# Optimization experiments

Measured on AMD Instinct MI355X. Metric: run time of the kernel, lower is better.

The kernel has to match this reference:

```python
import jax, jax.numpy as jnp
import numpy as np

B, L, C, H, W = 2, 3, 64, 32, 32
DI, N, DT_RANK, K = 128, 16, 4, 4  # d_inner=2*C, d_state, dt_rank=ceil(C/16), 4 scan dirs


def setup_inputs() -> dict:
    key = jax.random.key(0)
    ks = iter(jax.random.split(key, 48))
    nrm = lambda shape, s=0.02: jax.random.normal(next(ks), shape, jnp.float32) * s
    return {
        "image_sequence": jax.random.normal(next(ks), (B, L, C, H, W), jnp.float32),
        "difficult_zone": jax.random.normal(next(ks), (B, C, H, W), jnp.float32),
        "sigma": jax.random.uniform(next(ks), (B, C, H, W), jnp.float32),
        # LayerNorm2d applied to each frame
        "norm_g": jnp.ones((C,)), "norm_b": jnp.zeros((C,)),
        # ConvolutionalResBlock (in=3C -> out=C), GroupNorm(num_groups=1)
        "gn1_g": jnp.ones((3 * C,)), "gn1_b": jnp.zeros((3 * C,)),
        "conv1_w": nrm((C, 3 * C, 3, 3)), "conv1_b": jnp.zeros((C,)),
        "gn2_g": jnp.ones((C,)), "gn2_b": jnp.zeros((C,)),
        "conv2_w": nrm((C, C, 3, 3)), "conv2_b": jnp.zeros((C,)),
        "skip_w": nrm((C, 3 * C, 1, 1)), "skip_b": jnp.zeros((C,)),
        # VSSBlock pre-norms
        "ln1_g": jnp.ones((C,)), "ln1_b": jnp.zeros((C,)),
        "ln2_g": jnp.ones((C,)), "ln2_b": jnp.zeros((C,)),
        # SS2D
        "in_proj_w": nrm((2 * DI, C)),
        "dwconv_w": nrm((DI, 1, 3, 3)), "dwconv_b": jnp.zeros((DI,)),
        "x_proj_w": nrm((K, DT_RANK + 2 * N, DI)),
        "dt_proj_w": nrm((K, DI, DT_RANK), 0.1),
        "dt_proj_b": jnp.log(jnp.expm1(jnp.full((K, DI), 0.01, jnp.float32))),
        "A_logs": jnp.log(jnp.tile(jnp.arange(1, N + 1, dtype=jnp.float32), (K * DI, 1))),
        "Ds": jnp.ones((K * DI,)),
        "out_norm_g": jnp.ones((DI,)), "out_norm_b": jnp.zeros((DI,)),
        "out_proj_w": nrm((C, DI)),
        # Mlp (hidden = C)
        "fc1_w": nrm((C, C)), "fc1_b": jnp.zeros((C,)),
        "fc2_w": nrm((C, C)), "fc2_b": jnp.zeros((C,)),
    }


def _ln(x, g, b, eps=1e-5):  # layernorm over last axis
    m = x.mean(-1, keepdims=True)
    v = x.var(-1, keepdims=True)
    return (x - m) * jax.lax.rsqrt(v + eps) * g + b


def _ln2d(x, g, b, eps=1e-6):  # per-pixel channel layernorm, NCHW
    m = x.mean(1, keepdims=True)
    v = x.var(1, keepdims=True)
    return (x - m) * jax.lax.rsqrt(v + eps) * g[None, :, None, None] + b[None, :, None, None]


def _gn1(x, g, b, eps=1e-5):  # GroupNorm(num_groups=1), NCHW
    m = x.mean((1, 2, 3), keepdims=True)
    v = x.var((1, 2, 3), keepdims=True)
    return (x - m) * jax.lax.rsqrt(v + eps) * g[None, :, None, None] + b[None, :, None, None]


def _conv(x, w, b, pad):
    y = jax.lax.conv_general_dilated(x, w, (1, 1), [(pad, pad), (pad, pad)],
                                     dimension_numbers=("NCHW", "OIHW", "NCHW"))
    return y + b[None, :, None, None]


def _forward(image_sequence, difficult_zone, sigma, norm_g, norm_b, gn1_g, gn1_b,
             conv1_w, conv1_b, gn2_g, gn2_b, conv2_w, conv2_b, skip_w, skip_b,
             ln1_g, ln1_b, ln2_g, ln2_b, in_proj_w, dwconv_w, dwconv_b, x_proj_w,
             dt_proj_w, dt_proj_b, A_logs, Ds, out_norm_g, out_norm_b, out_proj_w,
             fc1_w, fc1_b, fc2_w, fc2_b):
    b, l, c, h, w = image_sequence.shape
    bl, L2 = b * l, h * w
    # fold frame loop into batch (identical math per frame in the torch loop)
    frames = _ln2d(image_sequence.reshape(bl, c, h, w), norm_g, norm_b)
    dz = jnp.broadcast_to(difficult_zone[:, None], (b, l, c, h, w)).reshape(bl, c, h, w)
    sg = jnp.broadcast_to(sigma[:, None], (b, l, c, h, w)).reshape(bl, c, h, w)
    x = jnp.concatenate([dz, frames, sg], axis=1)  # [bl, 3c, h, w]
    # channel compressor: pre-act conv res block
    hdn = _conv(jax.nn.silu(_gn1(x, gn1_g, gn1_b)), conv1_w, conv1_b, 1)
    hdn = _conv(jax.nn.silu(_gn1(hdn, gn2_g, gn2_b)), conv2_w, conv2_b, 1)
    x = hdn + _conv(x, skip_w, skip_b, 0)          # [bl, c, h, w]
    x = x.transpose(0, 2, 3, 1)                    # [bl, h, w, c]
    # --- VSSBlock (pre-norm): x = x + SS2D(LN(x)) ---
    xn = _ln(x, ln1_g, ln1_b)
    xz = xn @ in_proj_w.T                          # [bl,h,w,2*DI]
    xc, z = jnp.split(xz, 2, axis=-1)
    xc = xc.transpose(0, 3, 1, 2)                  # [bl, DI, h, w]
    xc = jax.lax.conv_general_dilated(xc, dwconv_w, (1, 1), [(1, 1), (1, 1)],
                                      dimension_numbers=("NCHW", "OIHW", "NCHW"),
                                      feature_group_count=DI) + dwconv_b[None, :, None, None]
    xc = jax.nn.silu(xc)
    # 4-direction scan inputs (HW, WH, and their reverses)
    xf = xc.reshape(bl, DI, L2)
    xt = xc.transpose(0, 1, 3, 2).reshape(bl, DI, L2)
    xs = jnp.stack([xf, xt], axis=1)
    xs = jnp.concatenate([xs, jnp.flip(xs, axis=-1)], axis=1)  # [bl, 4, DI, L2]
    x_dbl = jnp.einsum("bkdl,kcd->bkcl", xs, x_proj_w)
    dts, Bs, Cs = jnp.split(x_dbl, [DT_RANK, DT_RANK + N], axis=2)
    dts = jnp.einsum("bkrl,kdr->bkdl", dts, dt_proj_w) + dt_proj_b[None, :, :, None]
    dts = jax.nn.softplus(dts)                     # [bl, 4, DI, L2]
    A = -jnp.exp(A_logs).reshape(K, DI, N)
    dA = jnp.exp(dts[..., None] * A[None, :, :, None, :])            # [bl,4,DI,L2,N]
    dBu = dts[..., None] * Bs.transpose(0, 1, 3, 2)[:, :, None] * xs[..., None]
    a_t = dA.transpose(3, 0, 1, 2, 4)              # [L2, bl, 4, DI, N]
    bu_t = dBu.transpose(3, 0, 1, 2, 4)
    c_t = Cs.transpose(3, 0, 1, 2)                 # [L2, bl, 4, N]

    def step(hid, inp):
        a_i, bu_i, c_i = inp
        hid = a_i * hid + bu_i
        return hid, jnp.einsum("bkdn,bkn->bkd", hid, c_i)

    h0 = jnp.zeros((bl, K, DI, N), xs.dtype)
    _, ys = jax.lax.scan(step, h0, (a_t, bu_t, c_t))                 # [L2, bl, 4, DI]
    ys = ys.transpose(1, 2, 3, 0) + xs * Ds.reshape(K, DI)[None, :, :, None]
    inv = jnp.flip(ys[:, 2:4], axis=-1)
    y = (ys[:, 0] + inv[:, 0]
         + ys[:, 1].reshape(bl, DI, w, h).transpose(0, 1, 3, 2).reshape(bl, DI, L2)
         + inv[:, 1].reshape(bl, DI, w, h).transpose(0, 1, 3, 2).reshape(bl, DI, L2))
    y = _ln(y.transpose(0, 2, 1), out_norm_g, out_norm_b).reshape(bl, h, w, DI)
    y = y * jax.nn.silu(z)
    x = x + y @ out_proj_w.T
    # --- x = x + Mlp(LN(x)) ---
    xn = _ln(x, ln2_g, ln2_b)
    x = x + (jax.nn.gelu(xn @ fc1_w.T + fc1_b, approximate=False) @ fc2_w.T + fc2_b)
    return x.transpose(0, 3, 1, 2).reshape(b, l, c, h, w)


def reference(image_sequence, difficult_zone, sigma, norm_g, norm_b, gn1_g, gn1_b,
              conv1_w, conv1_b, gn2_g, gn2_b, conv2_w, conv2_b, skip_w, skip_b,
              ln1_g, ln1_b, ln2_g, ln2_b, in_proj_w, dwconv_w, dwconv_b, x_proj_w,
              dt_proj_w, dt_proj_b, A_logs, Ds, out_norm_g, out_norm_b, out_proj_w,
              fc1_w, fc1_b, fc2_w, fc2_b):
    return _forward(image_sequence, difficult_zone, sigma, norm_g, norm_b, gn1_g, gn1_b,
                    conv1_w, conv1_b, gn2_g, gn2_b, conv2_w, conv2_b, skip_w, skip_b,
                    ln1_g, ln1_b, ln2_g, ln2_b, in_proj_w, dwconv_w, dwconv_b, x_proj_w,
                    dt_proj_w, dt_proj_b, A_logs, Ds, out_norm_g, out_norm_b, out_proj_w,
                    fc1_w, fc1_b, fc2_w, fc2_b)
```

## Files before the change

kernel.cpp:

```cpp
#include <hip/hip_runtime.h>
#include <math.h>

#define BL    6
#define CCH   64
#define C3    192
#define L2    1024
#define DIC   128
#define NST   16
#define K4    4
#define PSTR  1088
#define NCH   32

#define LOG2E 1.44269504088896340736f
#define LN2C  0.69314718055994530942f

__device__ __forceinline__ float fexp(float x){ return __builtin_amdgcn_exp2f(x*LOG2E); }
__device__ __forceinline__ float fsilu(float x){ return x * __builtin_amdgcn_rcpf(1.f + fexp(-x)); }
__device__ __forceinline__ float fsoftplus(float x){
  if (x > 20.f) return x;
  return __builtin_amdgcn_logf(1.f + fexp(x)) * LN2C;
}
__device__ __forceinline__ float fgelu(float x){
  return 0.5f*x*(1.f + erff(x*0.70710678118654752440f));
}

__global__ __launch_bounds__(256) void k_ln2d(const float* __restrict__ img,
    const float* __restrict__ dz, const float* __restrict__ sg,
    const float* __restrict__ g, const float* __restrict__ b, float* __restrict__ x3c,
    float* __restrict__ psum1, float* __restrict__ psq1){
  __shared__ float ps[4][16], pq[4][16], gs[4], gq[4];
  int s = blockIdx.x >> 6;
  int pg = blockIdx.x & 63;
  int tid = threadIdx.x;
  int px = tid & 15; int cg = tid >> 4;
  int wv = tid >> 6; int lane = tid & 63;
  int p = pg*16 + px;
  int bsmp = s/3;
  const float* fr = img + (size_t)s*CCH*L2;
  float vals[4]; float sm=0.f, sq=0.f;
  #pragma unroll
  for (int j=0;j<4;++j){
    int c = cg*4 + j;
    float v = fr[c*L2 + p];
    vals[j]=v; sm+=v; sq+=v*v;
  }
  sm += __shfl_xor(sm,16,64); sq += __shfl_xor(sq,16,64);
  sm += __shfl_xor(sm,32,64); sq += __shfl_xor(sq,32,64);
  if (lane < 16){ ps[wv][lane]=sm; pq[wv][lane]=sq; }
  __syncthreads();
  sm = ps[0][px]+ps[1][px]+ps[2][px]+ps[3][px];
  sq = pq[0][px]+pq[1][px]+pq[2][px]+pq[3][px];
  float mean = sm*(1.f/CCH); float var = sq*(1.f/CCH)-mean*mean;
  float rs = rsqrtf(var + 1e-6f);
  float* o = x3c + (size_t)s*C3*L2;
  const float* dzp = dz + (size_t)bsmp*CCH*L2;
  const float* sgp = sg + (size_t)bsmp*CCH*L2;
  float gsm=0.f, gsq=0.f;
  #pragma unroll
  for (int j=0;j<4;++j){
    int c = cg*4+j;
    float dzv = dzp[c*L2+p];
    float nv  = (vals[j]-mean)*rs*g[c] + b[c];
    float sgv = sgp[c*L2+p];
    o[c*L2+p] = dzv;
    o[(CCH+c)*L2+p] = nv;
    o[(2*CCH+c)*L2+p] = sgv;
    gsm += dzv+nv+sgv; gsq += dzv*dzv+nv*nv+sgv*sgv;
  }
  for (int m=1;m<64;m<<=1){ gsm+=__shfl_xor(gsm,m,64); gsq+=__shfl_xor(gsq,m,64); }
  if (lane==0){ gs[wv]=gsm; gq[wv]=gsq; }
  __syncthreads();
  if (tid==0){
    psum1[blockIdx.x] = gs[0]+gs[1]+gs[2]+gs[3];
    psq1 [blockIdx.x] = gq[0]+gq[1]+gq[2]+gq[3];
  }
}

__global__ __launch_bounds__(256) void k_gnact_pad(const float* __restrict__ x,
    const float* __restrict__ psum, const float* __restrict__ psq,
    const float* __restrict__ g, const float* __restrict__ b,
    int ch, int parts, float inv_n, float eps, float* __restrict__ out){
  int bx = blockIdx.x;
  int s = bx / ch; int c = bx % ch;
  int tid = threadIdx.x;
  float sm=0.f, sq=0.f;
  for (int i=0;i<parts;++i){ sm += psum[s*parts+i]; sq += psq[s*parts+i]; }
  float mean = sm*inv_n;
  float var = sq*inv_n - mean*mean;
  float rs = rsqrtf(var + eps);
  float gc = g[c]*rs; float bc = b[c] - mean*rs*g[c];
  float4 v = *(const float4*)(x + (size_t)bx*1024 + tid*4);
  float4 o; o.x = fsilu(v.x*gc+bc); o.y = fsilu(v.y*gc+bc);
  o.z = fsilu(v.z*gc+bc); o.w = fsilu(v.w*gc+bc);
  float* pl = out + (size_t)bx*PSTR;
  *(float4*)(pl + 32 + tid*4) = o;
  float4 z4 = make_float4(0.f,0.f,0.f,0.f);
  if (tid < 8)  *(float4*)(pl + tid*4) = z4;
  else if (tid < 16) *(float4*)(pl + 1056 + (tid-8)*4) = z4;
}

__device__ __forceinline__ void conv_row_acc(float4& a0, float4& a1, float4 mid, float lf, float rt,
    const float* wp0, const float* wp1){
  float w0=wp0[0], w1=wp0[1], w2=wp0[2];
  a0.x = fmaf(w0,lf,   fmaf(w1,mid.x, fmaf(w2,mid.y, a0.x)));
  a0.y = fmaf(w0,mid.x,fmaf(w1,mid.y, fmaf(w2,mid.z, a0.y)));
  a0.z = fmaf(w0,mid.y,fmaf(w1,mid.z, fmaf(w2,mid.w, a0.z)));
  a0.w = fmaf(w0,mid.z,fmaf(w1,mid.w, fmaf(w2,rt,    a0.w)));
  float v0=wp1[0], v1=wp1[1], v2=wp1[2];
  a1.x = fmaf(v0,lf,   fmaf(v1,mid.x, fmaf(v2,mid.y, a1.x)));
  a1.y = fmaf(v0,mid.x,fmaf(v1,mid.y, fmaf(v2,mid.z, a1.y)));
  a1.z = fmaf(v0,mid.y,fmaf(v1,mid.z, fmaf(v2,mid.w, a1.z)));
  a1.w = fmaf(v0,mid.z,fmaf(v1,mid.w, fmaf(v2,rt,    a1.w)));
}

__device__ __forceinline__ void conv_ci_body(float4 m0, float4 m1, float4 m2, int q,
    const float* wp0, const float* wp1, float4& a0, float4& a1){
  float lf0=__shfl_up(m0.w,1,64), rt0=__shfl_down(m0.x,1,64);
  float lf1=__shfl_up(m1.w,1,64), rt1=__shfl_down(m1.x,1,64);
  float lf2=__shfl_up(m2.w,1,64), rt2=__shfl_down(m2.x,1,64);
  if (q==0){ lf0=0.f; lf1=0.f; lf2=0.f; }
  if (q==7){ rt0=0.f; rt1=0.f; rt2=0.f; }
  conv_row_acc(a0,a1,m0,lf0,rt0, wp0+0, wp1+0);
  conv_row_acc(a0,a1,m1,lf1,rt1, wp0+3, wp1+3);
  conv_row_acc(a0,a1,m2,lf2,rt2, wp0+6, wp1+6);
}

__global__ __launch_bounds__(256) void k_conv1_split(const float* __restrict__ xact,
    const float* __restrict__ w, float* __restrict__ part){
  int bx = blockIdx.x; int kk = bx&7; int cop=(bx>>3)&31; int s=bx>>8;
  int co0 = cop*2, co1 = co0+1;
  int tid = threadIdx.x; int row = tid>>3; int q = tid&7; int col0 = q*4;
  float4 a0 = make_float4(0.f,0.f,0.f,0.f);
  float4 a1 = make_float4(0.f,0.f,0.f,0.f);
  int ci0 = kk*24;
  const float* pl = xact + ((size_t)s*C3 + ci0)*PSTR + row*32 + col0;
  const float* wp0 = w + (size_t)(co0*C3 + ci0)*9;
  const float* wp1 = w + (size_t)(co1*C3 + ci0)*9;
  float4 m0 = *(const float4*)(pl);
  float4 m1 = *(const float4*)(pl+32);
  float4 m2 = *(const float4*)(pl+64);
  #pragma unroll 2
  for (int i=0;i<24;++i){
    const float* pn = pl + (i<23 ? PSTR : 0);
    float4 n0 = *(const float4*)(pn);
    float4 n1 = *(const float4*)(pn+32);
    float4 n2 = *(const float4*)(pn+64);
    conv_ci_body(m0,m1,m2,q, wp0, wp1, a0, a1);
    wp0 += 9; wp1 += 9; pl = pn; m0=n0; m1=n1; m2=n2;
  }
  float* pp = part + (size_t)kk*(BL*CCH*L2) + ((size_t)s*CCH+co0)*L2 + row*32+col0;
  *(float4*)pp = a0;
  *(float4*)(pp+L2) = a1;
}

__global__ __launch_bounds__(256) void k_reduce1(const float* __restrict__ part,
    const float* __restrict__ bias, float* __restrict__ h1,
    float* __restrict__ psum2, float* __restrict__ psq2){
  int co = blockIdx.x & 63; int s = blockIdx.x >> 6;
  size_t ofs = ((size_t)s*CCH+co)*L2 + threadIdx.x*4;
  const size_t stride = (size_t)BL*CCH*L2;
  float4 acc = *(const float4*)(part + ofs);
  #pragma unroll
  for (int kk=1;kk<8;++kk){
    float4 r = *(const float4*)(part + (size_t)kk*stride + ofs);
    acc.x += r.x; acc.y += r.y; acc.z += r.z; acc.w += r.w;
  }
  float bv = bias[co];
  acc.x += bv; acc.y += bv; acc.z += bv; acc.w += bv;
  *(float4*)(h1 + ofs) = acc;
  float sm = acc.x+acc.y+acc.z+acc.w;
  float sq = acc.x*acc.x+acc.y*acc.y+acc.z*acc.z+acc.w*acc.w;
  for (int m=1;m<64;m<<=1){ sm+=__shfl_xor(sm,m,64); sq+=__shfl_xor(sq,m,64); }
  __shared__ float s_sm[4], s_sq[4];
  int wv = threadIdx.x>>6;
  if ((threadIdx.x&63)==0){ s_sm[wv]=sm; s_sq[wv]=sq; }
  __syncthreads();
  if (threadIdx.x==0){
    psum2[blockIdx.x] = s_sm[0]+s_sm[1]+s_sm[2]+s_sm[3];
    psq2 [blockIdx.x] = s_sq[0]+s_sq[1]+s_sq[2]+s_sq[3];
  }
}

__global__ __launch_bounds__(256) void k_conv2_split(const float* __restrict__ xact2,
    const float* __restrict__ x3c, const float* __restrict__ w2,
    const float* __restrict__ wsk, float* __restrict__ part){
  int t = blockIdx.x; int role = t % 6; t /= 6;
  int cop = t & 31; int s = t >> 5;
  int co0 = cop*2, co1 = co0+1;
  int tid = threadIdx.x; int row = tid>>3; int q = tid&7; int col0 = q*4;
  int p = row*32+col0;
  float4 a0 = make_float4(0.f,0.f,0.f,0.f);
  float4 a1 = make_float4(0.f,0.f,0.f,0.f);
  if (role < 4){
    int ci0 = role*16;
    const float* pl = xact2 + ((size_t)s*CCH + ci0)*PSTR + row*32 + col0;
    const float* wp0 = w2 + (size_t)(co0*CCH + ci0)*9;
    const float* wp1 = w2 + (size_t)(co1*CCH + ci0)*9;
    float4 m0 = *(const float4*)(pl);
    float4 m1 = *(const float4*)(pl+32);
    float4 m2 = *(const float4*)(pl+64);
    #pragma unroll 2
    for (int i=0;i<16;++i){
      const float* pn = pl + (i<15 ? PSTR : 0);
      float4 n0 = *(const float4*)(pn);
      float4 n1 = *(const float4*)(pn+32);
      float4 n2 = *(const float4*)(pn+64);
      conv_ci_body(m0,m1,m2,q, wp0, wp1, a0, a1);
      wp0 += 9; wp1 += 9; pl = pn; m0=n0; m1=n1; m2=n2;
    }
  } else {
    int ci0 = (role-4)*96;
    const float* x3 = x3c + ((size_t)s*C3 + ci0)*L2 + p;
    const float* w0p = wsk + co0*C3 + ci0;
    const float* w1p = wsk + co1*C3 + ci0;
    #pragma unroll 4
    for (int ci=0; ci<96; ++ci){
      float4 v = *(const float4*)(x3 + (size_t)ci*L2);
      float ws0 = w0p[ci], ws1 = w1p[ci];
      a0.x = fmaf(ws0,v.x,a0.x); a0.y = fmaf(ws0,v.y,a0.y); a0.z = fmaf(ws0,v.z,a0.z); a0.w = fmaf(ws0,v.w,a0.w);
      a1.x = fmaf(ws1,v.x,a1.x); a1.y = fmaf(ws1,v.y,a1.y); a1.z = fmaf(ws1,v.z,a1.z); a1.w = fmaf(ws1,v.w,a1.w);
    }
  }
  float* pp = part + (size_t)role*(BL*CCH*L2) + ((size_t)s*CCH+co0)*L2 + p;
  *(float4*)pp = a0;
  *(float4*)(pp+L2) = a1;
}

__global__ __launch_bounds__(256) void k_red2_ln1_inproj(const float* __restrict__ part,
    const float* __restrict__ b2, const float* __restrict__ bsk,
    const float* __restrict__ g, const float* __restrict__ b,
    const float* __restrict__ W,
    float* __restrict__ x_cmaj, float* __restrict__ xc, float* __restrict__ z_t){
  __shared__ float xn_s[64*65];
  int bx = blockIdx.x; int oq = bx & 7; int pg = (bx>>3)&15; int s = bx>>7;
  int p0 = pg*64;
  int tid = threadIdx.x;
  const size_t stride = (size_t)BL*CCH*L2;
  #pragma unroll
  for (int kq=0;kq<4;++kq){
    int f = kq*256 + tid;
    int co = f >> 4; int px4 = (f & 15)*4;
    size_t ofs = ((size_t)s*CCH+co)*L2 + p0 + px4;
    float4 r0 = *(const float4*)(part + ofs);
    float4 r1 = *(const float4*)(part + stride + ofs);
    float4 r2 = *(const float4*)(part + 2*stride + ofs);
    float4 r3 = *(const float4*)(part + 3*stride + ofs);
    float4 r4 = *(const float4*)(part + 4*stride + ofs);
    float4 r5 = *(const float4*)(part + 5*stride + ofs);
    float bv = b2[co]+bsk[co];
    float4 o;
    o.x = ((r0.x+r1.x)+(r2.x+r3.x))+(r4.x+r5.x)+bv;
    o.y = ((r0.y+r1.y)+(r2.y+r3.y))+(r4.y+r5.y)+bv;
    o.z = ((r0.z+r1.z)+(r2.z+r3.z))+(r4.z+r5.z)+bv;
    o.w = ((r0.w+r1.w)+(r2.w+r3.w))+(r4.w+r5.w)+bv;
    if (oq == 0) *(float4*)(x_cmaj + ofs) = o;
    xn_s[(px4+0)*65 + co] = o.x;
    xn_s[(px4+1)*65 + co] = o.y;
    xn_s[(px4+2)*65 + co] = o.z;
    xn_s[(px4+3)*65 + co] = o.w;
  }
  __syncthreads();
  {
    int wv = __builtin_amdgcn_readfirstlane(tid>>6); int lane = tid&63;
    for (int j=0;j<16;++j){
      int pl = wv*16 + j;
      float v = xn_s[pl*65 + lane];
      float sm = v, sq = v*v;
      for (int m=1;m<64;m<<=1){ sm += __shfl_xor(sm,m,64); sq += __shfl_xor(sq,m,64); }
      float mean = sm*(1.f/64.f); float var = sq*(1.f/64.f) - mean*mean;
      float rs = rsqrtf(var + 1e-5f);
      xn_s[pl*65 + lane] = (v-mean)*rs*g[lane] + b[lane];
    }
  }
  __syncthreads();
  int px_l = tid & 63;
  int og = __builtin_amdgcn_readfirstlane(tid >> 6);
  int o0 = oq*32 + og*8;
  float acc[8];
  #pragma unroll
  for (int oi=0;oi<8;++oi) acc[oi]=0.f;
  for (int c=0;c<64;++c){
    float xv = xn_s[px_l*65 + c];
    #pragma unroll
    for (int oi=0;oi<8;++oi) acc[oi] = fmaf(W[(o0+oi)*64 + c], xv, acc[oi]);
  }
  int p = p0 + px_l;
  if (oq < 4){
    #pragma unroll
    for (int oi=0;oi<8;++oi) xc[((size_t)s*DIC + o0 + oi)*L2 + p] = acc[oi];
  } else {
    #pragma unroll
    for (int oi=0;oi<8;++oi) z_t[((size_t)s*DIC + (o0-128) + oi)*L2 + p] = acc[oi];
  }
}

__global__ __launch_bounds__(256) void k_xproj_dt(const float* __restrict__ xc,
    const float* __restrict__ dww, const float* __restrict__ dwb,
    const float* __restrict__ W,
    float* __restrict__ dtr, float* __restrict__ Bp, float* __restrict__ Cp,
    float* __restrict__ u_t){
  __shared__ float smem[128*68];
  int bx = blockIdx.x; int pg = bx & 15; int sk = bx >> 4;
  int k = sk & 3; int s = sk >> 2;
  int tid = threadIdx.x;
  for (int i = tid; i < 128*16; i += 256){
    int dr = i>>4; int j4 = (i&15)*4;
    int rw = j4>>5; int col0 = j4 & 31;
    int gr = pg*2 + rw;
    int q = i&7;
    const float* xr = xc + ((size_t)s*DIC+dr)*L2;
    const float* wp = dww + dr*9;
    float bv = dwb[dr];
    float4 acc = make_float4(bv,bv,bv,bv);
    #pragma unroll
    for (int dy=-1;dy<=1;++dy){
      int r = gr+dy;
      float4 mid = make_float4(0.f,0.f,0.f,0.f);
      if (0<=r && r<32) mid = *(const float4*)(xr + r*32 + col0);
      float lf = __shfl_up(mid.w,1,64); if(q==0) lf=0.f;
      float rt = __shfl_down(mid.x,1,64); if(q==7) rt=0.f;
      float w0=wp[(dy+1)*3], w1=wp[(dy+1)*3+1], w2=wp[(dy+1)*3+2];
      acc.x = fmaf(w0,lf,   fmaf(w1,mid.x, fmaf(w2,mid.y, acc.x)));
      acc.y = fmaf(w0,mid.x,fmaf(w1,mid.y, fmaf(w2,mid.z, acc.y)));
      acc.z = fmaf(w0,mid.y,fmaf(w1,mid.z, fmaf(w2,mid.w, acc.z)));
      acc.w = fmaf(w0,mid.z,fmaf(w1,mid.w, fmaf(w2,rt,    acc.w)));
    }
    acc.x = fsilu(acc.x); acc.y = fsilu(acc.y); acc.z = fsilu(acc.z); acc.w = fsilu(acc.w);
    *(float4*)&smem[dr*68 + j4] = acc;
  }
  __syncthreads();
  if (k == 0){
    float* ub = u_t + ((size_t)(s*L2) + pg*64)*DIC;
    for (int i = tid; i < 64*128; i += 256){
      int px2 = i>>7; int dd = i&127;
      ub[(size_t)px2*DIC + dd] = smem[dd*68 + px2];
    }
  }
  int px = tid & 63;
  int cgrp = __builtin_amdgcn_readfirstlane(tid >> 6);
  int c0 = cgrp*9;
  const float* wb = W + (size_t)(k*36 + c0)*DIC;
  float acc[9];
  #pragma unroll
  for (int ci=0;ci<9;++ci) acc[ci]=0.f;
  for (int d=0; d<DIC; ++d){
    float xv = smem[d*68 + px];
    #pragma unroll
    for (int ci=0;ci<9;++ci) acc[ci] = fmaf(wb[ci*DIC+d], xv, acc[ci]);
  }
  __syncthreads();
  #pragma unroll
  for (int ci=0;ci<9;++ci) smem[(c0+ci)*68 + px] = acc[ci];
  __syncthreads();
  {
    int pp = tid >> 2; int r = tid & 3;
    dtr[((size_t)sk*L2 + pg*64 + pp)*4 + r] = smem[r*68 + pp];
  }
  float* Bb = Bp + ((size_t)sk*L2 + pg*64)*NST;
  float* Cb = Cp + ((size_t)sk*L2 + pg*64)*NST;
  for (int i = tid; i < 1024; i += 256){
    int pp = i>>4; int n = i&15;
    Bb[pp*NST + n] = smem[(4+n)*68 + pp];
    Cb[pp*NST + n] = smem[(20+n)*68 + pp];
  }
}

__device__ __forceinline__ int scan_pix32(int ch, int j, int k){
  if (k==0) return ch*32 + j;
  if (k==1) return j*32 + ch;
  if (k==2) return 1023 - (ch*32 + j);
  return 1023 - (j*32 + ch);
}

struct StepH { float4 dt4; float uv; float4 B0,B1; };
__device__ __forceinline__ StepH loadH(const float* dr, const float* ub, const float* Bb, int p){
  StepH r;
  r.dt4 = *(const float4*)(dr + (size_t)p*4);
  r.uv = ub[(size_t)p*DIC];
  const float* bp = Bb + p*NST;
  r.B0 = *(const float4*)bp; r.B1 = *(const float4*)(bp+4);
  return r;
}
__device__ __forceinline__ float dt_eval(float4 w4, float bb, float4 d4){
  return fsoftplus(fmaf(w4.x,d4.x,fmaf(w4.y,d4.y,fmaf(w4.z,d4.z,fmaf(w4.w,d4.w,bb)))));
}

__global__ __launch_bounds__(256,4) void k_scan_part3(const float* __restrict__ dtr,
    const float* __restrict__ dtw, const float* __restrict__ dtb,
    const float* __restrict__ u_t, const float* __restrict__ Bp,
    const float* __restrict__ A_logs, float* __restrict__ hend, float* __restrict__ Ssum){
  int bx = blockIdx.x; int ch = bx & 31; int sk = bx >> 5;
  int k = sk & 3; int s = sk >> 2;
  int tid = threadIdx.x; int d = tid >> 1; int nh = tid & 1;
  float aco[8];
  {
    const float* ab = A_logs + (size_t)(k*DIC+d)*NST + nh*8;
    #pragma unroll
    for (int n=0;n<8;++n) aco[n] = -LOG2E * fexp(ab[n]);
  }
  float4 w4 = *(const float4*)(dtw + (size_t)(k*DIC+d)*4);
  float bb = dtb[k*DIC+d];
  float h[8]; float Sacc = 0.f;
  #pragma unroll
  for (int n=0;n<8;++n) h[n]=0.f;
  const float* dr = dtr + (size_t)sk*L2*4;
  const float* ub = u_t + (size_t)s*L2*DIC + d;
  const float* Bb = Bp + (size_t)sk*L2*NST + nh*8;
  StepH cur = loadH(dr, ub, Bb, scan_pix32(ch, 0, k));
  #pragma unroll 4
  for (int j=0;j<32;++j){
    StepH nxt;
    if (j < 31) nxt = loadH(dr, ub, Bb, scan_pix32(ch, j+1, k));
    float dtv = dt_eval(w4, bb, cur.dt4);
    Sacc += dtv;
    float tv = dtv*cur.uv;
    #define PSTEP(NI, BV) { float a_ = __builtin_amdgcn_exp2f(dtv*aco[NI]); \
      h[NI] = fmaf(a_, h[NI], tv*(BV)); }
    PSTEP(0,cur.B0.x) PSTEP(1,cur.B0.y) PSTEP(2,cur.B0.z) PSTEP(3,cur.B0.w)
    PSTEP(4,cur.B1.x) PSTEP(5,cur.B1.y) PSTEP(6,cur.B1.z) PSTEP(7,cur.B1.w)
    #undef PSTEP
    cur = nxt;
  }
  size_t base = ((size_t)(sk*NCH + ch)*DIC + d)*NST + nh*8;
  *(float4*)(hend + base)     = make_float4(h[0],h[1],h[2],h[3]);
  *(float4*)(hend + base + 4) = make_float4(h[4],h[5],h[6],h[7]);
  if (nh == 0) Ssum[(size_t)(sk*NCH + ch)*DIC + d] = Sacc;
}

__global__ __launch_bounds__(256) void k_scan_fix3(const float* __restrict__ hend,
    const float* __restrict__ Ssum, const float* __restrict__ A_logs,
    float* __restrict__ Hin){
  int t = blockIdx.x*256 + threadIdx.x;
  int n = t & 15; int d = (t>>4) & 127; int sk = t >> 11; int k = sk & 3;
  float aco = -LOG2E * fexp(A_logs[(size_t)(k*DIC+d)*NST + n]);
  float H = 0.f;
  #pragma unroll 8
  for (int ch=0; ch<NCH; ++ch){
    size_t sidx = (size_t)(sk*NCH + ch)*DIC + d;
    float pa = __builtin_amdgcn_exp2f(aco * Ssum[sidx]);
    float he = hend[sidx*NST + n];
    Hin[sidx*NST + n] = H;
    H = fmaf(pa, H, he);
  }
}

__global__ __launch_bounds__(256,4) void k_scan_y3(const float* __restrict__ dtr,
    const float* __restrict__ dtw, const float* __restrict__ dtb,
    const float* __restrict__ u_t, const float* __restrict__ Bp, const float* __restrict__ Cp,
    const float* __restrict__ A_logs, const float* __restrict__ Ds,
    const float* __restrict__ Hin, float* __restrict__ ys_t){
  int bx = blockIdx.x; int ch = bx & 31; int sk = bx >> 5;
  int k = sk & 3; int s = sk >> 2;
  int tid = threadIdx.x; int d = tid >> 1; int nh = tid & 1;
  float aco[8];
  {
    const float* ab = A_logs + (size_t)(k*DIC+d)*NST + nh*8;
    #pragma unroll
    for (int n=0;n<8;++n) aco[n] = -LOG2E * fexp(ab[n]);
  }
  float4 w4 = *(const float4*)(dtw + (size_t)(k*DIC+d)*4);
  float bb = dtb[k*DIC+d];
  float Dv = Ds[k*DIC+d];
  float h[8];
  size_t hbase = ((size_t)(sk*NCH + ch)*DIC + d)*NST + nh*8;
  {
    float4 h0 = *(const float4*)(Hin + hbase);
    float4 h1 = *(const float4*)(Hin + hbase + 4);
    h[0]=h0.x; h[1]=h0.y; h[2]=h0.z; h[3]=h0.w;
    h[4]=h1.x; h[5]=h1.y; h[6]=h1.z; h[7]=h1.w;
  }
  const float* dr = dtr + (size_t)sk*L2*4;
  const float* ub = u_t + (size_t)s*L2*DIC + d;
  const float* Bb = Bp + (size_t)sk*L2*NST + nh*8;
  const float* Cb = Cp + (size_t)sk*L2*NST + nh*8;
  float* yb = ys_t + (size_t)sk*L2*DIC + d;
  int pcur = scan_pix32(ch, 0, k);
  StepH cur = loadH(dr, ub, Bb, pcur);
  float4 Cc0 = *(const float4*)(Cb + pcur*NST);
  float4 Cc1 = *(const float4*)(Cb + pcur*NST + 4);
  #pragma unroll 4
  for (int j=0;j<32;++j){
    StepH nxt; float4 Cn0, Cn1; int pn = pcur;
    if (j < 31){
      pn = scan_pix32(ch, j+1, k);
      nxt = loadH(dr, ub, Bb, pn);
      Cn0 = *(const float4*)(Cb + pn*NST);
      Cn1 = *(const float4*)(Cb + pn*NST + 4);
    }
    float dtv = dt_eval(w4, bb, cur.dt4);
    float tv = dtv*cur.uv;
    float y0=0.f, y1=0.f, y2=0.f, y3=0.f;
    #define YSTEP(NI, BV, CV, YA) { float a_ = __builtin_amdgcn_exp2f(dtv*aco[NI]); \
      h[NI] = fmaf(a_, h[NI], tv*(BV)); YA = fmaf(h[NI], (CV), YA); }
    YSTEP(0,cur.B0.x,Cc0.x,y0) YSTEP(1,cur.B0.y,Cc0.y,y1) YSTEP(2,cur.B0.z,Cc0.z,y2) YSTEP(3,cur.B0.w,Cc0.w,y3)
    YSTEP(4,cur.B1.x,Cc1.x,y0) YSTEP(5,cur.B1.y,Cc1.y,y1) YSTEP(6,cur.B1.z,Cc1.z,y2) YSTEP(7,cur.B1.w,Cc1.w,y3)
    #undef YSTEP
    float py = (y0+y1)+(y2+y3);
    float tot = py + __shfl_xor(py, 1, 64);
    if (nh == 0) yb[(size_t)pcur*DIC] = fmaf(cur.uv, Dv, tot);
    cur = nxt; Cc0 = Cn0; Cc1 = Cn1; pcur = pn;
  }
}

__global__ __launch_bounds__(256) void k_tail(const float* __restrict__ ys_t,
    const float* __restrict__ z_t, const float* __restrict__ ong, const float* __restrict__ onb,
    const float* __restrict__ Wop, const float* __restrict__ x_cmaj,
    const float* __restrict__ g2, const float* __restrict__ b2n,
    const float* __restrict__ w1, const float* __restrict__ b1,
    const float* __restrict__ w2, const float* __restrict__ b2,
    float* __restrict__ out){
  __shared__ float yt[128*17];
  __shared__ float xvt[64*17];
  __shared__ float ts[64*17];
  int s = blockIdx.x >> 6; int pg = blockIdx.x & 63;
  int tid = threadIdx.x;
  {
    int wv = __builtin_amdgcn_readfirstlane(tid>>6); int lane = tid&63;
    int d0 = lane, d1 = lane+64;
    for (int i=0;i<4;++i){
      int px = i*4 + wv; int p = pg*16 + px;
      const float* yb = ys_t + ((size_t)(s*4)*L2 + p)*DIC;
      float ya = yb[d0] + yb[(size_t)L2*DIC + d0] + yb[(size_t)2*L2*DIC + d0] + yb[(size_t)3*L2*DIC + d0];
      float yc = yb[d1] + yb[(size_t)L2*DIC + d1] + yb[(size_t)2*L2*DIC + d1] + yb[(size_t)3*L2*DIC + d1];
      float sm = ya+yc, sq = ya*ya+yc*yc;
      for (int m=1;m<64;m<<=1){ sm+=__shfl_xor(sm,m,64); sq+=__shfl_xor(sq,m,64); }
      float mean = sm*(1.f/128.f); float var = sq*(1.f/128.f)-mean*mean;
      float rs = rsqrtf(var + 1e-5f);
      float yn0 = (ya-mean)*rs*ong[d0] + onb[d0];
      float yn1 = (yc-mean)*rs*ong[d1] + onb[d1];
      float zv0 = z_t[((size_t)s*DIC+d0)*L2 + p];
      float zv1 = z_t[((size_t)s*DIC+d1)*L2 + p];
      yt[d0*17 + px] = yn0 * fsilu(zv0);
      yt[d1*17 + px] = yn1 * fsilu(zv1);
    }
  }
  __syncthreads();
  {
    int px = tid & 15; int cgp = tid >> 4;
    int c0 = cgp*4;
    float a0=0.f,a1=0.f,a2=0.f,a3=0.f;
    for (int d=0; d<DIC; ++d){
      float yv = yt[d*17 + px];
      a0 = fmaf(Wop[(c0+0)*DIC + d], yv, a0);
      a1 = fmaf(Wop[(c0+1)*DIC + d], yv, a1);
      a2 = fmaf(Wop[(c0+2)*DIC + d], yv, a2);
      a3 = fmaf(Wop[(c0+3)*DIC + d], yv, a3);
    }
    int p = pg*16 + px;
    size_t base = ((size_t)s*CCH + c0)*L2 + p;
    xvt[(c0+0)*17 + px] = x_cmaj[base]      + a0;
    xvt[(c0+1)*17 + px] = x_cmaj[base+L2]   + a1;
    xvt[(c0+2)*17 + px] = x_cmaj[base+2*L2] + a2;
    xvt[(c0+3)*17 + px] = x_cmaj[base+3*L2] + a3;
  }
  __syncthreads();
  int px = tid & 15; int cgp = tid >> 4;
  float sm=0.f, sq=0.f;
  for (int c=0;c<64;++c){ float v = xvt[c*17+px]; sm+=v; sq+=v*v; }
  float mean = sm*(1.f/64.f);
  float rs = rsqrtf(sq*(1.f/64.f) - mean*mean + 1e-5f);
  int o0 = cgp*4;
  float t[4];
  #pragma unroll
  for (int oi=0;oi<4;++oi) t[oi] = b1[o0+oi];
  for (int c=0;c<64;++c){
    float xn = (xvt[c*17+px]-mean)*rs*g2[c] + b2n[c];
    #pragma unroll
    for (int oi=0;oi<4;++oi) t[oi] = fmaf(xn, w1[(o0+oi)*64 + c], t[oi]);
  }
  #pragma unroll
  for (int oi=0;oi<4;++oi) ts[(o0+oi)*17 + px] = fgelu(t[oi]);
  __syncthreads();
  int c0 = cgp*4;
  float acc[4];
  #pragma unroll
  for (int ci=0;ci<4;++ci) acc[ci] = xvt[(c0+ci)*17+px] + b2[c0+ci];
  for (int o=0;o<64;++o){
    float tv = ts[o*17+px];
    #pragma unroll
    for (int ci=0;ci<4;++ci) acc[ci] = fmaf(tv, w2[(c0+ci)*64 + o], acc[ci]);
  }
  int p = pg*16 + px;
  #pragma unroll
  for (int ci=0;ci<4;++ci) out[((size_t)s*CCH + c0+ci)*L2 + p] = acc[ci];
}

extern "C" void kernel_launch(void* const* d_in, const int* in_sizes, int n_in,
                              void* d_out, int out_size, void* d_ws, size_t ws_size,
                              hipStream_t stream){
  (void)in_sizes; (void)n_in; (void)out_size; (void)ws_size;
  const float* img      = (const float*)d_in[0];
  const float* dz       = (const float*)d_in[1];
  const float* sg       = (const float*)d_in[2];
  const float* norm_g   = (const float*)d_in[3];
  const float* norm_b   = (const float*)d_in[4];
  const float* gn1_g    = (const float*)d_in[5];
  const float* gn1_b    = (const float*)d_in[6];
  const float* conv1_w  = (const float*)d_in[7];
  const float* conv1_b  = (const float*)d_in[8];
  const float* gn2_g    = (const float*)d_in[9];
  const float* gn2_b    = (const float*)d_in[10];
  const float* conv2_w  = (const float*)d_in[11];
  const float* conv2_b  = (const float*)d_in[12];
  const float* skip_w   = (const float*)d_in[13];
  const float* skip_b   = (const float*)d_in[14];
  const float* ln1_g    = (const float*)d_in[15];
  const float* ln1_b    = (const float*)d_in[16];
  const float* ln2_g    = (const float*)d_in[17];
  const float* ln2_b    = (const float*)d_in[18];
  const float* in_proj_w= (const float*)d_in[19];
  const float* dwconv_w = (const float*)d_in[20];
  const float* dwconv_b = (const float*)d_in[21];
  const float* x_proj_w = (const float*)d_in[22];
  const float* dt_proj_w= (const float*)d_in[23];
  const float* dt_proj_b= (const float*)d_in[24];
  const float* A_logs   = (const float*)d_in[25];
  const float* Ds       = (const float*)d_in[26];
  const float* out_norm_g = (const float*)d_in[27];
  const float* out_norm_b = (const float*)d_in[28];
  const float* out_proj_w = (const float*)d_in[29];
  const float* fc1_w    = (const float*)d_in[30];
  const float* fc1_b    = (const float*)d_in[31];
  const float* fc2_w    = (const float*)d_in[32];
  const float* fc2_b    = (const float*)d_in[33];

  float* ws = (float*)d_ws;
  float* x3c    = ws;
  float* xact1  = x3c    + 1179648;
  float* h1     = xact1  + 1253376;
  float* xact2  = h1     + 393216;
  float* xpslot = xact2  + 417792;
  float* x_cmaj = xpslot + 393216;
  float* z_t    = x_cmaj + 393216;
  float* xc     = z_t    + 786432;
  float* cpslot = xc     + 786432;
  float* hole   = cpslot + 786432;
  float* scanbuf= hole   + 884736;
  float* ys_t   = scanbuf+ 3145728;
  float* statsb = ys_t   + 3145728;
  float* psum1  = statsb;
  float* psq1   = statsb + 384;
  float* psum2  = statsb + 768;
  float* psq2   = statsb + 1152;
  float* part1  = scanbuf;
  float* part2  = ys_t;
  float* hend   = x3c;
  float* u_t    = h1;
  float* Bp     = xpslot;
  float* Cp     = cpslot;
  float* dtr    = hole;
  float* Ssum   = hole + 98304;
  float* Hin    = scanbuf;

  k_ln2d<<<384, 256, 0, stream>>>(img, dz, sg, norm_g, norm_b, x3c, psum1, psq1);
  k_gnact_pad<<<6*C3, 256, 0, stream>>>(x3c, psum1, psq1, gn1_g, gn1_b, C3, 64,
                                        1.f/(C3*L2), 1e-5f, xact1);
  k_conv1_split<<<1536, 256, 0, stream>>>(xact1, conv1_w, part1);
  k_reduce1<<<384, 256, 0, stream>>>(part1, conv1_b, h1, psum2, psq2);
  k_gnact_pad<<<6*CCH, 256, 0, stream>>>(h1, psum2, psq2, gn2_g, gn2_b, CCH, 64,
                                         1.f/(CCH*L2), 1e-5f, xact2);
  k_conv2_split<<<1152, 256, 0, stream>>>(xact2, x3c, conv2_w, skip_w, part2);
  k_red2_ln1_inproj<<<768, 256, 0, stream>>>(part2, conv2_b, skip_b, ln1_g, ln1_b, in_proj_w,
                                             x_cmaj, xc, z_t);
  k_xproj_dt<<<384, 256, 0, stream>>>(xc, dwconv_w, dwconv_b, x_proj_w, dtr, Bp, Cp, u_t);
  k_scan_part3<<<768, 256, 0, stream>>>(dtr, dt_proj_w, dt_proj_b, u_t, Bp, A_logs, hend, Ssum);
  k_scan_fix3<<<192, 256, 0, stream>>>(hend, Ssum, A_logs, Hin);
  k_scan_y3<<<768, 256, 0, stream>>>(dtr, dt_proj_w, dt_proj_b, u_t, Bp, Cp, A_logs, Ds, Hin, ys_t);
  k_tail<<<384, 256, 0, stream>>>(ys_t, z_t, out_norm_g, out_norm_b, out_proj_w, x_cmaj,
                                  ln2_g, ln2_b, fc1_w, fc1_b, fc2_w, fc2_b, (float*)d_out);
}
```

Before: 291.2 us.

## Move skip 1x1 conv into GN1 kernel and widen grids of several kernels

The 1x1 skip convolution moves out of the conv2 kernel into a merged kernel alongside the GN1 activation/padding, so it runs earlier, in parallel with other work. Conv1 is split 12 ways over input channels instead of 8, and the reduce loop grows to match. The LN2d and tail kernels process 8 pixels per block instead of 16, which doubles their block counts. The goal is more parallelism and shorter per-block work on the many CUs, at the cost of more partial-sum traffic in conv1 and less weight reuse per thread in the tail.

```diff
diff --git a/kernel.cpp b/kernel.cpp
--- a/kernel.cpp
+++ b/kernel.cpp
@@ -28,25 +28,26 @@
     const float* __restrict__ dz, const float* __restrict__ sg,
     const float* __restrict__ g, const float* __restrict__ b, float* __restrict__ x3c,
     float* __restrict__ psum1, float* __restrict__ psq1){
-  __shared__ float ps[4][16], pq[4][16], gs[4], gq[4];
-  int s = blockIdx.x >> 6;
-  int pg = blockIdx.x & 63;
+  __shared__ float ps[4][8], pq[4][8], gs[4], gq[4];
+  int s = blockIdx.x >> 7;
+  int pg = blockIdx.x & 127;
   int tid = threadIdx.x;
-  int px = tid & 15; int cg = tid >> 4;
+  int px = tid & 7; int cg = tid >> 3;
   int wv = tid >> 6; int lane = tid & 63;
-  int p = pg*16 + px;
+  int p = pg*8 + px;
   int bsmp = s/3;
   const float* fr = img + (size_t)s*CCH*L2;
-  float vals[4]; float sm=0.f, sq=0.f;
-  #pragma unroll
-  for (int j=0;j<4;++j){
-    int c = cg*4 + j;
+  float vals[2]; float sm=0.f, sq=0.f;
+  #pragma unroll
+  for (int j=0;j<2;++j){
+    int c = cg*2 + j;
     float v = fr[c*L2 + p];
     vals[j]=v; sm+=v; sq+=v*v;
   }
+  sm += __shfl_xor(sm,8,64);  sq += __shfl_xor(sq,8,64);
   sm += __shfl_xor(sm,16,64); sq += __shfl_xor(sq,16,64);
   sm += __shfl_xor(sm,32,64); sq += __shfl_xor(sq,32,64);
-  if (lane < 16){ ps[wv][lane]=sm; pq[wv][lane]=sq; }
+  if (lane < 8){ ps[wv][lane]=sm; pq[wv][lane]=sq; }
   __syncthreads();
   sm = ps[0][px]+ps[1][px]+ps[2][px]+ps[3][px];
   sq = pq[0][px]+pq[1][px]+pq[2][px]+pq[3][px];
@@ -57,8 +58,8 @@
   const float* sgp = sg + (size_t)bsmp*CCH*L2;
   float gsm=0.f, gsq=0.f;
   #pragma unroll
-  for (int j=0;j<4;++j){
-    int c = cg*4+j;
+  for (int j=0;j<2;++j){
+    int c = cg*2+j;
     float dzv = dzp[c*L2+p];
     float nv  = (vals[j]-mean)*rs*g[c] + b[c];
     float sgv = sgp[c*L2+p];
@@ -73,6 +74,54 @@
   if (tid==0){
     psum1[blockIdx.x] = gs[0]+gs[1]+gs[2]+gs[3];
     psq1 [blockIdx.x] = gq[0]+gq[1]+gq[2]+gq[3];
+  }
+}
+
+__global__ __launch_bounds__(256) void k_gnact1_skip(const float* __restrict__ x3c,
+    const float* __restrict__ psum, const float* __restrict__ psq,
+    const float* __restrict__ g, const float* __restrict__ b,
+    const float* __restrict__ wsk,
+    float* __restrict__ xact1, float* __restrict__ part){
+  int bx = blockIdx.x;
+  int tid = threadIdx.x;
+  if (bx < 1152){
+    int s = bx / C3; int c = bx % C3;
+    float sm=0.f, sq=0.f;
+    for (int i=0;i<128;++i){ sm += psum[s*128+i]; sq += psq[s*128+i]; }
+    float mean = sm*(1.f/(C3*L2));
+    float var = sq*(1.f/(C3*L2)) - mean*mean;
+    float rs = rsqrtf(var + 1e-5f);
+    float gc = g[c]*rs; float bc = b[c] - mean*rs*g[c];
+    float4 v = *(const float4*)(x3c + (size_t)bx*1024 + tid*4);
+    float4 o; o.x = fsilu(v.x*gc+bc); o.y = fsilu(v.y*gc+bc);
+    o.z = fsilu(v.z*gc+bc); o.w = fsilu(v.w*gc+bc);
+    float* pl = xact1 + (size_t)bx*PSTR;
+    *(float4*)(pl + 32 + tid*4) = o;
+    float4 z4 = make_float4(0.f,0.f,0.f,0.f);
+    if (tid < 8)  *(float4*)(pl + tid*4) = z4;
+    else if (tid < 16) *(float4*)(pl + 1056 + (tid-8)*4) = z4;
+  } else {
+    int t = bx - 1152;
+    int role = t & 1; int cop = (t>>1)&31; int s = t >> 6;
+    int co0 = cop*2, co1 = co0+1;
+    int row = tid>>3; int q = tid&7; int col0 = q*4;
+    int p = row*32+col0;
+    float4 a0 = make_float4(0.f,0.f,0.f,0.f);
+    float4 a1 = make_float4(0.f,0.f,0.f,0.f);
+    int ci0 = role*96;
+    const float* x3 = x3c + ((size_t)s*C3 + ci0)*L2 + p;
+    const float* w0p = wsk + co0*C3 + ci0;
+    const float* w1p = wsk + co1*C3 + ci0;
+    #pragma unroll 4
+    for (int ci=0; ci<96; ++ci){
+      float4 v = *(const float4*)(x3 + (size_t)ci*L2);
+      float ws0 = w0p[ci], ws1 = w1p[ci];
+      a0.x = fmaf(ws0,v.x,a0.x); a0.y = fmaf(ws0,v.y,a0.y); a0.z = fmaf(ws0,v.z,a0.z); a0.w = fmaf(ws0,v.w,a0.w);
+      a1.x = fmaf(ws1,v.x,a1.x); a1.y = fmaf(ws1,v.y,a1.y); a1.z = fmaf(ws1,v.z,a1.z); a1.w = fmaf(ws1,v.w,a1.w);
+    }
+    float* pp = part + (size_t)(4+role)*(BL*CCH*L2) + ((size_t)s*CCH+co0)*L2 + p;
+    *(float4*)pp = a0;
+    *(float4*)(pp+L2) = a1;
   }
 }
 
@@ -127,12 +176,13 @@
 
 __global__ __launch_bounds__(256) void k_conv1_split(const float* __restrict__ xact,
     const float* __restrict__ w, float* __restrict__ part){
-  int bx = blockIdx.x; int kk = bx&7; int cop=(bx>>3)&31; int s=bx>>8;
+  int bx = blockIdx.x; int kk = bx % 12; int r = bx / 12;
+  int cop = r & 31; int s = r >> 5;
   int co0 = cop*2, co1 = co0+1;
   int tid = threadIdx.x; int row = tid>>3; int q = tid&7; int col0 = q*4;
   float4 a0 = make_float4(0.f,0.f,0.f,0.f);
   float4 a1 = make_float4(0.f,0.f,0.f,0.f);
-  int ci0 = kk*24;
+  int ci0 = kk*16;
   const float* pl = xact + ((size_t)s*C3 + ci0)*PSTR + row*32 + col0;
   const float* wp0 = w + (size_t)(co0*C3 + ci0)*9;
   const float* wp1 = w + (size_t)(co1*C3 + ci0)*9;
@@ -140,8 +190,8 @@
   float4 m1 = *(const float4*)(pl+32);
   float4 m2 = *(const float4*)(pl+64);
   #pragma unroll 2
-  for (int i=0;i<24;++i){
-    const float* pn = pl + (i<23 ? PSTR : 0);
+  for (int i=0;i<16;++i){
+    const float* pn = pl + (i<15 ? PSTR : 0);
     float4 n0 = *(const float4*)(pn);
     float4 n1 = *(const float4*)(pn+32);
     float4 n2 = *(const float4*)(pn+64);
@@ -161,7 +211,7 @@
   const size_t stride = (size_t)BL*CCH*L2;
   float4 acc = *(const float4*)(part + ofs);
   #pragma unroll
-  for (int kk=1;kk<8;++kk){
+  for (int kk=1;kk<12;++kk){
     float4 r = *(const float4*)(part + (size_t)kk*stride + ofs);
     acc.x += r.x; acc.y += r.y; acc.z += r.z; acc.w += r.w;
   }
@@ -182,44 +232,29 @@
 }
 
 __global__ __launch_bounds__(256) void k_conv2_split(const float* __restrict__ xact2,
-    const float* __restrict__ x3c, const float* __restrict__ w2,
-    const float* __restrict__ wsk, float* __restrict__ part){
-  int t = blockIdx.x; int role = t % 6; t /= 6;
+    const float* __restrict__ w2, float* __restrict__ part){
+  int bx = blockIdx.x; int role = bx & 3; int t = bx >> 2;
   int cop = t & 31; int s = t >> 5;
   int co0 = cop*2, co1 = co0+1;
   int tid = threadIdx.x; int row = tid>>3; int q = tid&7; int col0 = q*4;
   int p = row*32+col0;
   float4 a0 = make_float4(0.f,0.f,0.f,0.f);
   float4 a1 = make_float4(0.f,0.f,0.f,0.f);
-  if (role < 4){
-    int ci0 = role*16;
-    const float* pl = xact2 + ((size_t)s*CCH + ci0)*PSTR + row*32 + col0;
-    const float* wp0 = w2 + (size_t)(co0*CCH + ci0)*9;
-    const float* wp1 = w2 + (size_t)(co1*CCH + ci0)*9;
-    float4 m0 = *(const float4*)(pl);
-    float4 m1 = *(const float4*)(pl+32);
-    float4 m2 = *(const float4*)(pl+64);
-    #pragma unroll 2
-    for (int i=0;i<16;++i){
-      const float* pn = pl + (i<15 ? PSTR : 0);
-      float4 n0 = *(const float4*)(pn);
-      float4 n1 = *(const float4*)(pn+32);
-      float4 n2 = *(const float4*)(pn+64);
-      conv_ci_body(m0,m1,m2,q, wp0, wp1, a0, a1);
-      wp0 += 9; wp1 += 9; pl = pn; m0=n0; m1=n1; m2=n2;
-    }
-  } else {
-    int ci0 = (role-4)*96;
-    const float* x3 = x3c + ((size_t)s*C3 + ci0)*L2 + p;
-    const float* w0p = wsk + co0*C3 + ci0;
-    const float* w1p = wsk + co1*C3 + ci0;
-    #pragma unroll 4
-    for (int ci=0; ci<96; ++ci){
-      float4 v = *(const float4*)(x3 + (size_t)ci*L2);
-      float ws0 = w0p[ci], ws1 = w1p[ci];
-      a0.x = fmaf(ws0,v.x,a0.x); a0.y = fmaf(ws0,v.y,a0.y); a0.z = fmaf(ws0,v.z,a0.z); a0.w = fmaf(ws0,v.w,a0.w);
-      a1.x = fmaf(ws1,v.x,a1.x); a1.y = fmaf(ws1,v.y,a1.y); a1.z = fmaf(ws1,v.z,a1.z); a1.w = fmaf(ws1,v.w,a1.w);
-    }
+  int ci0 = role*16;
+  const float* pl = xact2 + ((size_t)s*CCH + ci0)*PSTR + row*32 + col0;
+  const float* wp0 = w2 + (size_t)(co0*CCH + ci0)*9;
+  const float* wp1 = w2 + (size_t)(co1*CCH + ci0)*9;
+  float4 m0 = *(const float4*)(pl);
+  float4 m1 = *(const float4*)(pl+32);
+  float4 m2 = *(const float4*)(pl+64);
+  #pragma unroll 2
+  for (int i=0;i<16;++i){
+    const float* pn = pl + (i<15 ? PSTR : 0);
+    float4 n0 = *(const float4*)(pn);
+    float4 n1 = *(const float4*)(pn+32);
+    float4 n2 = *(const float4*)(pn+64);
+    conv_ci_body(m0,m1,m2,q, wp0, wp1, a0, a1);
+    wp0 += 9; wp1 += 9; pl = pn; m0=n0; m1=n1; m2=n2;
   }
   float* pp = part + (size_t)role*(BL*CCH*L2) + ((size_t)s*CCH+co0)*L2 + p;
   *(float4*)pp = a0;
@@ -509,16 +544,16 @@
     const float* __restrict__ w1, const float* __restrict__ b1,
     const float* __restrict__ w2, const float* __restrict__ b2,
     float* __restrict__ out){
-  __shared__ float yt[128*17];
-  __shared__ float xvt[64*17];
-  __shared__ float ts[64*17];
-  int s = blockIdx.x >> 6; int pg = blockIdx.x & 63;
+  __shared__ float yt[128*9];
+  __shared__ float xvt[64*9];
+  __shared__ float ts[64*9];
+  int s = blockIdx.x >> 7; int pg = blockIdx.x & 127;
   int tid = threadIdx.x;
   {
     int wv = __builtin_amdgcn_readfirstlane(tid>>6); int lane = tid&63;
     int d0 = lane, d1 = lane+64;
-    for (int i=0;i<4;++i){
-      int px = i*4 + wv; int p = pg*16 + px;
+    for (int i=0;i<2;++i){
+      int px = i*4 + wv; int p = pg*8 + px;
       const float* yb = ys_t + ((size_t)(s*4)*L2 + p)*DIC;
       float ya = yb[d0] + yb[(size_t)L2*DIC + d0] + yb[(size_t)2*L2*DIC + d0] + yb[(size_t)3*L2*DIC + d0];
       float yc = yb[d1] + yb[(size_t)L2*DIC + d1] + yb[(size_t)2*L2*DIC + d1] + yb[(size_t)3*L2*DIC + d1];
@@ -530,59 +565,52 @@
       float yn1 = (yc-mean)*rs*ong[d1] + onb[d1];
       float zv0 = z_t[((size_t)s*DIC+d0)*L2 + p];
       float zv1 = z_t[((size_t)s*DIC+d1)*L2 + p];
-      yt[d0*17 + px] = yn0 * fsilu(zv0);
-      yt[d1*17 + px] = yn1 * fsilu(zv1);
+      yt[d0*9 + px] = yn0 * fsilu(zv0);
+      yt[d1*9 + px] = yn1 * fsilu(zv1);
     }
   }
   __syncthreads();
   {
-    int px = tid & 15; int cgp = tid >> 4;
-    int c0 = cgp*4;
-    float a0=0.f,a1=0.f,a2=0.f,a3=0.f;
+    int px = tid & 7; int cgp = tid >> 3;
+    int c0 = cgp*2;
+    float a0=0.f,a1=0.f;
     for (int d=0; d<DIC; ++d){
-      float yv = yt[d*17 + px];
+      float yv = yt[d*9 + px];
       a0 = fmaf(Wop[(c0+0)*DIC + d], yv, a0);
       a1 = fmaf(Wop[(c0+1)*DIC + d], yv, a1);
-      a2 = fmaf(Wop[(c0+2)*DIC + d], yv, a2);
-      a3 = fmaf(Wop[(c0+3)*DIC + d], yv, a3);
     }
-    int p = pg*16 + px;
+    int p = pg*8 + px;
     size_t base = ((size_t)s*CCH + c0)*L2 + p;
-    xvt[(c0+0)*17 + px] = x_cmaj[base]      + a0;
-    xvt[(c0+1)*17 + px] = x_cmaj[base+L2]   + a1;
-    xvt[(c0+2)*17 + px] = x_cmaj[base+2*L2] + a2;
-    xvt[(c0+3)*17 + px] = x_cmaj[base+3*L2] + a3;
-  }
-  __syncthreads();
-  int px = tid & 15; int cgp = tid >> 4;
+    xvt[(c0+0)*9 + px] = x_cmaj[base]    + a0;
+    xvt[(c0+1)*9 + px] = x_cmaj[base+L2] + a1;
+  }
+  __syncthreads();
+  int px = tid & 7; int cgp = tid >> 3;
   float sm=0.f, sq=0.f;
-  for (int c=0;c<64;++c){ float v = xvt[c*17+px]; sm+=v; sq+=v*v; }
+  for (int c=0;c<64;++c){ float v = xvt[c*9+px]; sm+=v; sq+=v*v; }
   float mean = sm*(1.f/64.f);
   float rs = rsqrtf(sq*(1.f/64.f) - mean*mean + 1e-5f);
-  int o0 = cgp*4;
-  float t[4];
-  #pragma unroll
-  for (int oi=0;oi<4;++oi) t[oi] = b1[o0+oi];
+  int o0 = cgp*2;
+  float t0 = b1[o0], t1 = b1[o0+1];
   for (int c=0;c<64;++c){
-    float xn = (xvt[c*17+px]-mean)*rs*g2[c] + b2n[c];
-    #pragma unroll
-    for (int oi=0;oi<4;++oi) t[oi] = fmaf(xn, w1[(o0+oi)*64 + c], t[oi]);
-  }
-  #pragma unroll
-  for (int oi=0;oi<4;++oi) ts[(o0+oi)*17 + px] = fgelu(t[oi]);
-  __syncthreads();
-  int c0 = cgp*4;
-  float acc[4];
-  #pragma unroll
-  for (int ci=0;ci<4;++ci) acc[ci] = xvt[(c0+ci)*17+px] + b2[c0+ci];
+    float xn = (xvt[c*9+px]-mean)*rs*g2[c] + b2n[c];
+    t0 = fmaf(xn, w1[(o0+0)*64 + c], t0);
+    t1 = fmaf(xn, w1[(o0+1)*64 + c], t1);
+  }
+  ts[(o0+0)*9 + px] = fgelu(t0);
+  ts[(o0+1)*9 + px] = fgelu(t1);
+  __syncthreads();
+  int c0 = cgp*2;
+  float acc0 = xvt[(c0+0)*9+px] + b2[c0+0];
+  float acc1 = xvt[(c0+1)*9+px] + b2[c0+1];
   for (int o=0;o<64;++o){
-    float tv = ts[o*17+px];
-    #pragma unroll
-    for (int ci=0;ci<4;++ci) acc[ci] = fmaf(tv, w2[(c0+ci)*64 + o], acc[ci]);
-  }
-  int p = pg*16 + px;
-  #pragma unroll
-  for (int ci=0;ci<4;++ci) out[((size_t)s*CCH + c0+ci)*L2 + p] = acc[ci];
+    float tv = ts[o*9+px];
+    acc0 = fmaf(tv, w2[(c0+0)*64 + o], acc0);
+    acc1 = fmaf(tv, w2[(c0+1)*64 + o], acc1);
+  }
+  int p = pg*8 + px;
+  out[((size_t)s*CCH + c0+0)*L2 + p] = acc0;
+  out[((size_t)s*CCH + c0+1)*L2 + p] = acc1;
 }
 
 extern "C" void kernel_launch(void* const* d_in, const int* in_sizes, int n_in,
@@ -639,9 +667,9 @@
   float* ys_t   = scanbuf+ 3145728;
   float* statsb = ys_t   + 3145728;
   float* psum1  = statsb;
-  float* psq1   = statsb + 384;
-  float* psum2  = statsb + 768;
-  float* psq2   = statsb + 1152;
+  float* psq1   = statsb + 768;
+  float* psum2  = statsb + 1536;
+  float* psq2   = statsb + 1920;
   float* part1  = scanbuf;
   float* part2  = ys_t;
   float* hend   = x3c;
@@ -652,20 +680,20 @@
   float* Ssum   = hole + 98304;
   float* Hin    = scanbuf;
 
-  k_ln2d<<<384, 256, 0, stream>>>(img, dz, sg, norm_g, norm_b, x3c, psum1, psq1);
-  k_gnact_pad<<<6*C3, 256, 0, stream>>>(x3c, psum1, psq1, gn1_g, gn1_b, C3, 64,
-                                        1.f/(C3*L2), 1e-5f, xact1);
-  k_conv1_split<<<1536, 256, 0, stream>>>(xact1, conv1_w, part1);
+  k_ln2d<<<768, 256, 0, stream>>>(img, dz, sg, norm_g, norm_b, x3c, psum1, psq1);
+  k_gnact1_skip<<<1536, 256, 0, stream>>>(x3c, psum1, psq1, gn1_g, gn1_b, skip_w,
+                                          xact1, part2);
+  k_conv1_split<<<2304, 256, 0, stream>>>(xact1, conv1_w, part1);
   k_reduce1<<<384, 256, 0, stream>>>(part1, conv1_b, h1, psum2, psq2);
   k_gnact_pad<<<6*CCH, 256, 0, stream>>>(h1, psum2, psq2, gn2_g, gn2_b, CCH, 64,
                                          1.f/(CCH*L2), 1e-5f, xact2);
-  k_conv2_split<<<1152, 256, 0, stream>>>(xact2, x3c, conv2_w, skip_w, part2);
+  k_conv2_split<<<768, 256, 0, stream>>>(xact2, conv2_w, part2);
   k_red2_ln1_inproj<<<768, 256, 0, stream>>>(part2, conv2_b, skip_b, ln1_g, ln1_b, in_proj_w,
                                              x_cmaj, xc, z_t);
   k_xproj_dt<<<384, 256, 0, stream>>>(xc, dwconv_w, dwconv_b, x_proj_w, dtr, Bp, Cp, u_t);
   k_scan_part3<<<768, 256, 0, stream>>>(dtr, dt_proj_w, dt_proj_b, u_t, Bp, A_logs, hend, Ssum);
   k_scan_fix3<<<192, 256, 0, stream>>>(hend, Ssum, A_logs, Hin);
   k_scan_y3<<<768, 256, 0, stream>>>(dtr, dt_proj_w, dt_proj_b, u_t, Bp, Cp, A_logs, Ds, Hin, ys_t);
-  k_tail<<<384, 256, 0, stream>>>(ys_t, z_t, out_norm_g, out_norm_b, out_proj_w, x_cmaj,
+  k_tail<<<768, 256, 0, stream>>>(ys_t, z_t, out_norm_g, out_norm_b, out_proj_w, x_cmaj,
                                   ln2_g, ln2_b, fc1_w, fc1_b, fc2_w, fc2_b, (float*)d_out);
 }
```

After: 286.7 us. Within noise of the previous version (-1.5%).
